# Optimization experiments

Measured on AMD Instinct MI355X. Metric: run time of the kernel, lower is better.

The kernel has to match this reference:

```python
import jax, jax.numpy as jnp
import numpy as np

N = 50000      # nodes
E = 1600000    # edges (avg degree 32)
F_IN = 256     # input feature dim
H = 128        # hidden == output size of GCN
C = 40         # num_class


def setup_inputs() -> dict:
    key = jax.random.key(0)
    ks = jax.random.split(key, 13)
    inp = {
        "features": jax.random.normal(ks[0], (N, F_IN), dtype=jnp.float32),
        "src": jax.random.randint(ks[1], (E,), 0, N, dtype=jnp.int32),
        "dst": jax.random.randint(ks[2], (E,), 0, N, dtype=jnp.int32),
        "edge_weight": jax.random.uniform(ks[3], (E,), dtype=jnp.float32),
        "y": jax.random.normal(ks[4], (N, C), dtype=jnp.float32),
        # GCN layer 1
        "W1": jax.random.normal(ks[5], (F_IN, H), dtype=jnp.float32) / np.sqrt(F_IN),
        "b1": jnp.zeros((H,), dtype=jnp.float32),
        # GCN layer 2
        "W2": jax.random.normal(ks[6], (H, H), dtype=jnp.float32) / np.sqrt(H),
        "b2": jnp.zeros((H,), dtype=jnp.float32),
        # y_fc_emb: Linear(num_class, output_size)
        "We": jax.random.normal(ks[7], (C, H), dtype=jnp.float32) / np.sqrt(C),
        "be": jnp.zeros((H,), dtype=jnp.float32),
        # y_fc: Linear(hidden*2, num_class)
        "Wf": jax.random.normal(ks[8], (2 * H, C), dtype=jnp.float32) / np.sqrt(2 * H),
        "bf": jnp.zeros((C,), dtype=jnp.float32),
    }
    return inp


def _spmm(edge_weight, src, dst, x, n):
    # (sparse adj) @ x : out[i] = sum_{(j->i)} w_ji * x[j]
    return jax.ops.segment_sum(edge_weight[:, None] * x[src], dst, num_segments=n)


def reference(features, src, dst, edge_weight, y, W1, b1, W2, b2, We, be, Wf, bf):
    n = features.shape[0]
    # F.normalize: L2 row-normalize with eps=1e-12 clamp
    norm = jnp.maximum(jnp.linalg.norm(features, axis=1, keepdims=True), 1e-12)
    x = features / norm
    # GCN layer 1: relu(adj @ (x @ W1) + b1)   (dropout = 0)
    h = jax.nn.relu(_spmm(edge_weight, src, dst, x @ W1, n) + b1)
    # GCN layer 2: adj @ (h @ W2) + b2
    h = _spmm(edge_weight, src, dst, h @ W2, n) + b2
    # label embedding + head
    y_emb = y @ We + be
    logits = jnp.concatenate([y_emb, h], axis=1) @ Wf + bf
    return jax.nn.softmax(logits, axis=-1)
```

## Files before the change

kernel.cpp:

```cpp
#include <hip/hip_runtime.h>
#include <hip/hip_bf16.h>
#include <hip/hip_fp16.h>
#include <cstdint>
#include <cstddef>
#include <cmath>

#define F_IN 256
#define HDIM 128
#define CCLS 40
#define NBMAX 1024
#define EPB_H 16384

typedef short bf16x8 __attribute__((ext_vector_type(8)));
typedef float f32x4 __attribute__((ext_vector_type(4)));

__device__ inline unsigned pkbf(float a, float b) {
  __hip_bfloat162 h = __float22bfloat162_rn(make_float2(a, b));
  unsigned u;
  __builtin_memcpy(&u, &h, 4);
  return u;
}
__device__ inline unsigned short bfr(float f) {
  __hip_bfloat16 h = __float2bfloat16(f);
  unsigned short u;
  __builtin_memcpy(&u, &h, 2);
  return u;
}
__device__ inline float f16tof(unsigned short hb) {
  __half hv;
  __builtin_memcpy(&hv, &hb, 2);
  return __half2float(hv);
}
__device__ inline unsigned short ftof16(float f) {
  __half hv = __float2half(f);
  unsigned short u;
  __builtin_memcpy(&u, &hv, 2);
  return u;
}

__global__ __launch_bounds__(256) void prep_kernel(const float* __restrict__ x,
                                                   unsigned short* __restrict__ featbf,
                                                   const float* __restrict__ W1,
                                                   const float* __restrict__ W2,
                                                   unsigned short* __restrict__ W1T,
                                                   unsigned short* __restrict__ W2T,
                                                   const float* __restrict__ We,
                                                   const float* __restrict__ be,
                                                   const float* __restrict__ Wf,
                                                   const float* __restrict__ bf,
                                                   float* __restrict__ Wc,
                                                   float* __restrict__ bc,
                                                   const int* __restrict__ dst,
                                                   int* __restrict__ gcount,
                                                   int n, int e, int nb) {
  const int b = blockIdx.x;
  const int t = threadIdx.x;
  const int nblk = (n + 15) >> 4;
  if (b < nblk) {
    const int wv = t >> 6, l = t & 63;
    const int r0 = b * 16 + wv * 4;
    const bool q0 = r0 < n, q1 = r0 + 1 < n, q2 = r0 + 2 < n, q3 = r0 + 3 < n;
    const float* p = x + (size_t)r0 * F_IN + l * 4;
    float4 z = make_float4(0.f, 0.f, 0.f, 0.f);
    float4 v0 = q0 ? *(const float4*)(p) : z;
    float4 v1 = q1 ? *(const float4*)(p + F_IN) : z;
    float4 v2 = q2 ? *(const float4*)(p + 2 * F_IN) : z;
    float4 v3 = q3 ? *(const float4*)(p + 3 * F_IN) : z;
    float s0 = v0.x * v0.x + v0.y * v0.y + v0.z * v0.z + v0.w * v0.w;
    float s1 = v1.x * v1.x + v1.y * v1.y + v1.z * v1.z + v1.w * v1.w;
    float s2 = v2.x * v2.x + v2.y * v2.y + v2.z * v2.z + v2.w * v2.w;
    float s3 = v3.x * v3.x + v3.y * v3.y + v3.z * v3.z + v3.w * v3.w;
#pragma unroll
    for (int off = 32; off; off >>= 1) {
      s0 += __shfl_xor(s0, off, 64);
      s1 += __shfl_xor(s1, off, 64);
      s2 += __shfl_xor(s2, off, 64);
      s3 += __shfl_xor(s3, off, 64);
    }
    float i0 = 1.0f / fmaxf(sqrtf(s0), 1e-12f);
    float i1 = 1.0f / fmaxf(sqrtf(s1), 1e-12f);
    float i2 = 1.0f / fmaxf(sqrtf(s2), 1e-12f);
    float i3 = 1.0f / fmaxf(sqrtf(s3), 1e-12f);
    unsigned short* o = featbf + (size_t)r0 * F_IN + l * 4;
    if (q0) *(uint2*)(o) = make_uint2(pkbf(v0.x * i0, v0.y * i0), pkbf(v0.z * i0, v0.w * i0));
    if (q1) *(uint2*)(o + F_IN) = make_uint2(pkbf(v1.x * i1, v1.y * i1), pkbf(v1.z * i1, v1.w * i1));
    if (q2) *(uint2*)(o + 2 * F_IN) = make_uint2(pkbf(v2.x * i2, v2.y * i2), pkbf(v2.z * i2, v2.w * i2));
    if (q3) *(uint2*)(o + 3 * F_IN) = make_uint2(pkbf(v3.x * i3, v3.y * i3), pkbf(v3.z * i3, v3.w * i3));
  } else if (b < nblk + 192) {
    int idx = (b - nblk) * 256 + t;
    if (idx < 128 * 256) {
      int nr = idx >> 8, k = idx & 255;
      W1T[idx] = bfr(W1[k * 128 + nr]);
    } else {
      int i2 = idx - 128 * 256;
      if (i2 < 128 * 128) {
        int nr = i2 >> 7, k = i2 & 127;
        W2T[i2] = bfr(W2[k * 128 + nr]);
      }
    }
  } else if (b < nblk + 194) {
    int part = b - (nblk + 192);
    int lo = part * 800, hi = lo + 800;
    for (int i = lo + t; i < hi; i += 256) {
      int c = i / CCLS, j = i % CCLS;
      float s = 0.f;
      for (int f = 0; f < HDIM; ++f) s += We[c * HDIM + f] * Wf[f * CCLS + j];
      Wc[i] = s;
    }
    if (part == 0 && t < CCLS) {
      float s = bf[t];
      for (int f = 0; f < HDIM; ++f) s += be[f] * Wf[f * CCLS + t];
      bc[t] = s;
    }
  } else {
    __shared__ int h[NBMAX];
    for (int i = t; i < nb; i += 256) h[i] = 0;
    __syncthreads();
    int b4 = (b - (nblk + 194)) * (EPB_H / 4);
#pragma unroll
    for (int k = 0; k < EPB_H / 1024; ++k) {
      int gi = b4 + k * 256 + t;
      int e0 = gi * 4;
      int4 d = make_int4(-1, -1, -1, -1);
      if (e0 + 3 < e) d = ((const int4*)dst)[gi];
      else if (e0 < e) {
        d.x = dst[e0];
        if (e0 + 1 < e) d.y = dst[e0 + 1];
        if (e0 + 2 < e) d.z = dst[e0 + 2];
      }
      if (d.x >= 0) atomicAdd(&h[d.x >> 6], 1);
      if (d.y >= 0) atomicAdd(&h[d.y >> 6], 1);
      if (d.z >= 0) atomicAdd(&h[d.z >> 6], 1);
      if (d.w >= 0) atomicAdd(&h[d.w >> 6], 1);
    }
    __syncthreads();
    for (int i = t; i < nb; i += 256)
      if (h[i]) atomicAdd(&gcount[i], h[i]);
  }
}

#define EPB 8192
__global__ __launch_bounds__(256) void bucket_scatter(const int* __restrict__ src,
                                                      const int* __restrict__ dst,
                                                      const float* __restrict__ w,
                                                      const int* __restrict__ gcount,
                                                      int* __restrict__ gcursor,
                                                      uint2* __restrict__ ews, int e, int nb) {
  __shared__ int hist[NBMAX];
  __shared__ int sb[NBMAX];
  __shared__ int lcur[NBMAX];
  __shared__ int part[256];
  const int t = threadIdx.x;
  for (int i = t; i < nb; i += 256) { hist[i] = 0; lcur[i] = 0; }
  __syncthreads();
  const int b4 = blockIdx.x * 2048;
  int4 dv[8];
#pragma unroll
  for (int k = 0; k < 8; ++k) {
    int gi = b4 + k * 256 + t;
    int e0 = gi * 4;
    int4 d = make_int4(-1, -1, -1, -1);
    if (e0 + 3 < e) d = ((const int4*)dst)[gi];
    else if (e0 < e) {
      d.x = dst[e0];
      if (e0 + 1 < e) d.y = dst[e0 + 1];
      if (e0 + 2 < e) d.z = dst[e0 + 2];
    }
    dv[k] = d;
    if (d.x >= 0) atomicAdd(&hist[d.x >> 6], 1);
    if (d.y >= 0) atomicAdd(&hist[d.y >> 6], 1);
    if (d.z >= 0) atomicAdd(&hist[d.z >> 6], 1);
    if (d.w >= 0) atomicAdd(&hist[d.w >> 6], 1);
  }
  __syncthreads();
  int v[4];
  int s = 0;
#pragma unroll
  for (int k = 0; k < 4; ++k) {
    int i = t * 4 + k;
    v[k] = (i < nb) ? gcount[i] : 0;
    s += v[k];
  }
  part[t] = s;
  __syncthreads();
  for (int off = 1; off < 256; off <<= 1) {
    int x = part[t];
    if (t >= off) x += part[t - off];
    __syncthreads();
    part[t] = x;
    __syncthreads();
  }
  int run = (t == 0) ? 0 : part[t - 1];
#pragma unroll
  for (int k = 0; k < 4; ++k) {
    int i = t * 4 + k;
    if (i < nb) sb[i] = run;
    run += v[k];
  }
  __syncthreads();
  for (int i = t; i < nb; i += 256) {
    int c = hist[i];
    sb[i] = sb[i] + (c ? atomicAdd(&gcursor[i], c) : 0);
  }
  __syncthreads();
#pragma unroll
  for (int k = 0; k < 8; ++k) {
    int gi = b4 + k * 256 + t;
    int e0 = gi * 4;
    if (e0 >= e) continue;
    int4 s4 = make_int4(0, 0, 0, 0);
    float4 w4 = make_float4(0.f, 0.f, 0.f, 0.f);
    if (e0 + 3 < e) { s4 = ((const int4*)src)[gi]; w4 = ((const float4*)w)[gi]; }
    else {
      s4.x = src[e0]; w4.x = w[e0];
      if (e0 + 1 < e) { s4.y = src[e0 + 1]; w4.y = w[e0 + 1]; }
      if (e0 + 2 < e) { s4.z = src[e0 + 2]; w4.z = w[e0 + 2]; }
    }
    int4 d = dv[k];
    if (d.x >= 0) { int bb = d.x >> 6; int r = atomicAdd(&lcur[bb], 1);
      ews[sb[bb] + r] = make_uint2(((unsigned)(d.x & 63) << 26) | (unsigned)s4.x, __float_as_uint(w4.x)); }
    if (d.y >= 0) { int bb = d.y >> 6; int r = atomicAdd(&lcur[bb], 1);
      ews[sb[bb] + r] = make_uint2(((unsigned)(d.y & 63) << 26) | (unsigned)s4.y, __float_as_uint(w4.y)); }
    if (d.z >= 0) { int bb = d.z >> 6; int r = atomicAdd(&lcur[bb], 1);
      ews[sb[bb] + r] = make_uint2(((unsigned)(d.z & 63) << 26) | (unsigned)s4.z, __float_as_uint(w4.z)); }
    if (d.w >= 0) { int bb = d.w >> 6; int r = atomicAdd(&lcur[bb], 1);
      ews[sb[bb] + r] = make_uint2(((unsigned)(d.w & 63) << 26) | (unsigned)s4.w, __float_as_uint(w4.w)); }
  }
}

__global__ __launch_bounds__(256) void bucket_sort(const uint2* __restrict__ ews,
                                                   const int* __restrict__ gcount,
                                                   unsigned* __restrict__ ews2,
                                                   int* __restrict__ row_off,
                                                   int n, int nb) {
  __shared__ int cnt64[64];
  __shared__ int cur[64];
  __shared__ int sred[4];
  const int t = threadIdx.x;
  const int b = blockIdx.x;
  int partial = 0;
  for (int i = t; i < b; i += 256) partial += gcount[i];
#pragma unroll
  for (int off = 32; off; off >>= 1) partial += __shfl_xor(partial, off, 64);
  if ((t & 63) == 0) sred[t >> 6] = partial;
  if (t < 64) cnt64[t] = 0;
  __syncthreads();
  const int e0 = sred[0] + sred[1] + sred[2] + sred[3];
  const int e1 = e0 + gcount[b];
  for (int i = e0 + t; i < e1; i += 256) atomicAdd(&cnt64[(unsigned)ews[i].x >> 26], 1);
  __syncthreads();
  if (t == 0) {
    int run = 0;
    for (int d = 0; d < 64; ++d) {
      int c = cnt64[d];
      cur[d] = run;
      run += c;
    }
  }
  __syncthreads();
  if (t < 64) {
    int node = b * 64 + t;
    if (node < n) row_off[node] = e0 + cur[t];
  }
  if (b == nb - 1 && t == 0) row_off[n] = e1;
  __syncthreads();
  for (int i = e0 + t; i < e1; i += 256) {
    uint2 p = ews[i];
    int d = (unsigned)p.x >> 26;
    int pos = e0 + atomicAdd(&cur[d], 1);
    unsigned rec = (p.x & 0xFFFFu) | ((unsigned)ftof16(__uint_as_float(p.y)) << 16);
    ews2[pos] = rec;
  }
}

#define SPMM_PAIR(ua, ub)                                                      \
  {                                                                            \
    unsigned u = half ? (ub) : (ua);                                           \
    float wt = f16tof((unsigned short)(u >> 16));                              \
    const uint2 xv = *(const uint2*)(xin + (size_t)(u & 0xFFFFu) * HDIM + fo); \
    acc.x = fmaf(wt, __uint_as_float(xv.x << 16), acc.x);                      \
    acc.y = fmaf(wt, __uint_as_float(xv.x & 0xFFFF0000u), acc.y);              \
    acc.z = fmaf(wt, __uint_as_float(xv.y << 16), acc.z);                      \
    acc.w = fmaf(wt, __uint_as_float(xv.y & 0xFFFF0000u), acc.w);              \
  }

template <int OUT_BF16>
__global__ __launch_bounds__(256) void spmm_bf16(const unsigned short* __restrict__ xin,
                                                 const unsigned* __restrict__ ews,
                                                 const int* __restrict__ row_off,
                                                 const float* __restrict__ bias,
                                                 void* __restrict__ outp, int n,
                                                 int do_relu) {
  const int t = threadIdx.x;
  const int l = t & 63;
  const int node = blockIdx.x * 4 + (t >> 6);
  if (node >= n) return;
  const int ue0 = __builtin_amdgcn_readfirstlane(row_off[node]);
  const int ue1 = __builtin_amdgcn_readfirstlane(row_off[node + 1]);
  const int cnt = ue1 - ue0;
  const unsigned* ep = ews + ue0;
  const int fo = (l & 31) * 4;
  const int half = l >> 5;
  float4 acc = make_float4(0.f, 0.f, 0.f, 0.f);

  int k = 0;
  for (; k + 16 <= cnt; k += 16) {
    unsigned a0 = ep[k + 0], a1 = ep[k + 1], a2 = ep[k + 2], a3 = ep[k + 3];
    unsigned a4 = ep[k + 4], a5 = ep[k + 5], a6 = ep[k + 6], a7 = ep[k + 7];
    unsigned a8 = ep[k + 8], a9 = ep[k + 9], a10 = ep[k + 10], a11 = ep[k + 11];
    unsigned a12 = ep[k + 12], a13 = ep[k + 13], a14 = ep[k + 14], a15 = ep[k + 15];
    SPMM_PAIR(a0, a1);
    SPMM_PAIR(a2, a3);
    SPMM_PAIR(a4, a5);
    SPMM_PAIR(a6, a7);
    SPMM_PAIR(a8, a9);
    SPMM_PAIR(a10, a11);
    SPMM_PAIR(a12, a13);
    SPMM_PAIR(a14, a15);
  }
  for (; k + 8 <= cnt; k += 8) {
    unsigned a0 = ep[k + 0], a1 = ep[k + 1], a2 = ep[k + 2], a3 = ep[k + 3];
    unsigned a4 = ep[k + 4], a5 = ep[k + 5], a6 = ep[k + 6], a7 = ep[k + 7];
    SPMM_PAIR(a0, a1);
    SPMM_PAIR(a2, a3);
    SPMM_PAIR(a4, a5);
    SPMM_PAIR(a6, a7);
  }
  for (; k < cnt; k += 2) {
    unsigned a0 = ep[k];
    unsigned a1 = (k + 1 < cnt) ? ep[k + 1] : 0u;
    SPMM_PAIR(a0, a1);
  }

  acc.x += __shfl_xor(acc.x, 32, 64);
  acc.y += __shfl_xor(acc.y, 32, 64);
  acc.z += __shfl_xor(acc.z, 32, 64);
  acc.w += __shfl_xor(acc.w, 32, 64);
  if (l < 32) {
    float4 bv = *(const float4*)(bias + fo);
    float4 r = make_float4(acc.x + bv.x, acc.y + bv.y, acc.z + bv.z, acc.w + bv.w);
    if (do_relu) {
      r.x = fmaxf(r.x, 0.f); r.y = fmaxf(r.y, 0.f);
      r.z = fmaxf(r.z, 0.f); r.w = fmaxf(r.w, 0.f);
    }
    if (OUT_BF16) {
      uint2 o = make_uint2(pkbf(r.x, r.y), pkbf(r.z, r.w));
      *(uint2*)((unsigned short*)outp + (size_t)node * HDIM + fo) = o;
    } else {
      *(float4*)((float*)outp + (size_t)node * HDIM + fo) = r;
    }
  }
}

template <int K>
__global__ __launch_bounds__(256) void gemm_mfma(const unsigned short* __restrict__ A,
                                                 const unsigned short* __restrict__ WT,
                                                 unsigned short* __restrict__ C, int M) {
  const int t = threadIdx.x;
  const int w = t >> 6, l = t & 63;
  const int ln = l & 15, quad = l >> 4;
  const int m0 = blockIdx.x * 64 + w * 16;
  const int arow = m0 + ln;
  const unsigned short* aptr = A + (size_t)(arow < M ? arow : (M - 1)) * K + quad * 8;

  f32x4 acc[8];
#pragma unroll
  for (int i = 0; i < 8; ++i) acc[i] = (f32x4){0.f, 0.f, 0.f, 0.f};

#pragma unroll
  for (int k0 = 0; k0 < K; k0 += 32) {
    bf16x8 af = *(const bf16x8*)(aptr + k0);
#pragma unroll
    for (int ti = 0; ti < 8; ++ti) {
      bf16x8 bf = *(const bf16x8*)(WT + (size_t)(ti * 16 + ln) * K + k0 + quad * 8);
      acc[ti] = __builtin_amdgcn_mfma_f32_16x16x32_bf16(af, bf, acc[ti], 0, 0, 0);
    }
  }

#pragma unroll
  for (int r = 0; r < 4; ++r) {
    int grow = m0 + quad * 4 + r;
    if (grow < M) {
      unsigned short* cp = C + (size_t)grow * HDIM + ln;
#pragma unroll
      for (int ti = 0; ti < 8; ++ti) cp[ti * 16] = bfr(acc[ti][r]);
    }
  }
}

__global__ __launch_bounds__(64) void head_kernel(const float* __restrict__ y,
                                                  const float* __restrict__ h2,
                                                  const float* __restrict__ Wc,
                                                  const float* __restrict__ bc,
                                                  const float* __restrict__ Wf,
                                                  float* __restrict__ out, int n) {
  __shared__ float sW[169 * CCLS];
  const int t = threadIdx.x;
  for (int i = t; i < 400; i += 64) ((float4*)sW)[i] = ((const float4*)Wc)[i];
  for (int i = t; i < 1280; i += 64)
    ((float4*)(sW + CCLS * CCLS))[i] = ((const float4*)(Wf + HDIM * CCLS))[i];
  if (t < 10) ((float4*)(sW + 168 * CCLS))[t] = ((const float4*)bc)[t];
  __syncthreads();

  const int node = blockIdx.x * 64 + t;
  const int nc = node < n ? node : n - 1;
  const float* zy = y + (size_t)nc * CCLS;
  const float* zh = h2 + (size_t)nc * HDIM;

  float acc[40];
#pragma unroll
  for (int cq = 0; cq < 10; ++cq) {
    float4 b4 = *(const float4*)&sW[168 * CCLS + cq * 4];
    acc[cq * 4 + 0] = b4.x; acc[cq * 4 + 1] = b4.y;
    acc[cq * 4 + 2] = b4.z; acc[cq * 4 + 3] = b4.w;
  }

#pragma unroll 2
  for (int kc = 0; kc < 10; ++kc) {
    float4 zv = *(const float4*)(zy + kc * 4);
    float zj[4] = {zv.x, zv.y, zv.z, zv.w};
#pragma unroll
    for (int j = 0; j < 4; ++j) {
      const float* wr = sW + (kc * 4 + j) * CCLS;
#pragma unroll
      for (int cq = 0; cq < 10; ++cq) {
        float4 w4 = *(const float4*)(wr + cq * 4);
        acc[cq * 4 + 0] = fmaf(zj[j], w4.x, acc[cq * 4 + 0]);
        acc[cq * 4 + 1] = fmaf(zj[j], w4.y, acc[cq * 4 + 1]);
        acc[cq * 4 + 2] = fmaf(zj[j], w4.z, acc[cq * 4 + 2]);
        acc[cq * 4 + 3] = fmaf(zj[j], w4.w, acc[cq * 4 + 3]);
      }
    }
  }
#pragma unroll 2
  for (int kc = 0; kc < 32; ++kc) {
    float4 zv = *(const float4*)(zh + kc * 4);
    float zj[4] = {zv.x, zv.y, zv.z, zv.w};
#pragma unroll
    for (int j = 0; j < 4; ++j) {
      const float* wr = sW + (40 + kc * 4 + j) * CCLS;
#pragma unroll
      for (int cq = 0; cq < 10; ++cq) {
        float4 w4 = *(const float4*)(wr + cq * 4);
        acc[cq * 4 + 0] = fmaf(zj[j], w4.x, acc[cq * 4 + 0]);
        acc[cq * 4 + 1] = fmaf(zj[j], w4.y, acc[cq * 4 + 1]);
        acc[cq * 4 + 2] = fmaf(zj[j], w4.z, acc[cq * 4 + 2]);
        acc[cq * 4 + 3] = fmaf(zj[j], w4.w, acc[cq * 4 + 3]);
      }
    }
  }

  float m = acc[0];
#pragma unroll
  for (int c = 1; c < 40; ++c) m = fmaxf(m, acc[c]);
  float sum = 0.f;
#pragma unroll
  for (int c = 0; c < 40; ++c) { acc[c] = __expf(acc[c] - m); sum += acc[c]; }
  float inv = 1.0f / sum;
  if (node < n) {
    float* op = out + (size_t)node * CCLS;
#pragma unroll
    for (int cq = 0; cq < 10; ++cq) {
      float4 o = make_float4(acc[cq * 4 + 0] * inv, acc[cq * 4 + 1] * inv,
                             acc[cq * 4 + 2] * inv, acc[cq * 4 + 3] * inv);
      *(float4*)(op + cq * 4) = o;
    }
  }
}

extern "C" void kernel_launch(void* const* d_in, const int* in_sizes, int n_in,
                              void* d_out, int out_size, void* d_ws, size_t ws_size,
                              hipStream_t stream) {
  (void)n_in; (void)out_size; (void)ws_size;
  const float* features = (const float*)d_in[0];
  const int*   src      = (const int*)d_in[1];
  const int*   dst      = (const int*)d_in[2];
  const float* ew       = (const float*)d_in[3];
  const float* y        = (const float*)d_in[4];
  const float* W1       = (const float*)d_in[5];
  const float* b1       = (const float*)d_in[6];
  const float* W2       = (const float*)d_in[7];
  const float* b2       = (const float*)d_in[8];
  const float* We       = (const float*)d_in[9];
  const float* be       = (const float*)d_in[10];
  const float* Wf       = (const float*)d_in[11];
  const float* bf       = (const float*)d_in[12];
  float* out = (float*)d_out;

  const int n = in_sizes[0] / F_IN;
  const int e = in_sizes[1];
  const int nb = (n + 63) >> 6;

  char* w = (char*)d_ws;
  auto take = [&](size_t bytes) {
    char* p = w;
    w += (bytes + 255) & ~(size_t)255;
    return p;
  };
  int*   gz       = (int*)take((size_t)2 * nb * 4);
  int*   gcount   = gz;
  int*   gcursor  = gz + nb;
  int*   row_off  = (int*)take((size_t)(n + 1) * 4);
  uint2* ews      = (uint2*)take((size_t)e * 8);
  unsigned* ews2  = (unsigned*)take((size_t)(e + 16) * 4);
  unsigned short* featbf = (unsigned short*)take((size_t)n * F_IN * 2);
  unsigned short* bufH1  = (unsigned short*)take((size_t)n * HDIM * 2);
  unsigned short* bufH2  = (unsigned short*)take((size_t)n * HDIM * 2);
  float* bufS     = (float*)take((size_t)n * HDIM * 4);
  unsigned short* W1T = (unsigned short*)take((size_t)HDIM * F_IN * 2);
  unsigned short* W2T = (unsigned short*)take((size_t)HDIM * HDIM * 2);
  float* Wc       = (float*)take(CCLS * CCLS * 4);
  float* bc       = (float*)take(CCLS * 4);

  const int nblk = (n + 15) >> 4;
  const int hb = (e + EPB_H - 1) / EPB_H;
  hipMemsetAsync(gz, 0, (size_t)2 * nb * 4, stream);
  prep_kernel<<<nblk + 194 + hb, 256, 0, stream>>>(features, featbf, W1, W2, W1T, W2T,
                                                   We, be, Wf, bf, Wc, bc, dst, gcount,
                                                   n, e, nb);
  bucket_scatter<<<(e + EPB - 1) / EPB, 256, 0, stream>>>(src, dst, ew, gcount, gcursor,
                                                          ews, e, nb);
  bucket_sort<<<nb, 256, 0, stream>>>(ews, gcount, ews2, row_off, n, nb);

  gemm_mfma<F_IN><<<(n + 63) / 64, 256, 0, stream>>>(featbf, W1T, bufH1, n);
  spmm_bf16<1><<<(n + 3) / 4, 256, 0, stream>>>(bufH1, ews2, row_off, b1, bufH2, n, 1);
  gemm_mfma<HDIM><<<(n + 63) / 64, 256, 0, stream>>>(bufH2, W2T, bufH1, n);
  spmm_bf16<0><<<(n + 3) / 4, 256, 0, stream>>>(bufH1, ews2, row_off, b2, bufS, n, 0);
  head_kernel<<<(n + 63) / 64, 64, 0, stream>>>(y, bufS, Wc, bc, Wf, out, n);
}
```

Before: 370.9 us.

## Fuse row normalization into first GEMM and widen SpMM gathers to 16B

Moves the L2 row normalization and bf16 conversion out of the prep kernel and into a new GEMM kernel that normalizes 64 rows into shared memory before running MFMA. This drops the write and re-read of the bf16 feature buffer. The SpMM kernel now gives each wave four 16-lane groups that each process a different edge with 8 features per lane (16-byte loads), unrolled 32 edges deep, and then reduces across the groups. This gives more gathers in flight and wider loads, at the cost of more registers and a two-step shuffle reduction. The fused GEMM has no __syncthreads between the shared-memory writes and reads, but each wave only reads the rows it wrote itself.

```diff
diff --git a/kernel.cpp b/kernel.cpp
--- a/kernel.cpp
+++ b/kernel.cpp
@@ -38,9 +38,7 @@
   return u;
 }
 
-__global__ __launch_bounds__(256) void prep_kernel(const float* __restrict__ x,
-                                                   unsigned short* __restrict__ featbf,
-                                                   const float* __restrict__ W1,
+__global__ __launch_bounds__(256) void prep_kernel(const float* __restrict__ W1,
                                                    const float* __restrict__ W2,
                                                    unsigned short* __restrict__ W1T,
                                                    unsigned short* __restrict__ W2T,
@@ -52,42 +50,11 @@
                                                    float* __restrict__ bc,
                                                    const int* __restrict__ dst,
                                                    int* __restrict__ gcount,
-                                                   int n, int e, int nb) {
+                                                   int e, int nb) {
   const int b = blockIdx.x;
   const int t = threadIdx.x;
-  const int nblk = (n + 15) >> 4;
-  if (b < nblk) {
-    const int wv = t >> 6, l = t & 63;
-    const int r0 = b * 16 + wv * 4;
-    const bool q0 = r0 < n, q1 = r0 + 1 < n, q2 = r0 + 2 < n, q3 = r0 + 3 < n;
-    const float* p = x + (size_t)r0 * F_IN + l * 4;
-    float4 z = make_float4(0.f, 0.f, 0.f, 0.f);
-    float4 v0 = q0 ? *(const float4*)(p) : z;
-    float4 v1 = q1 ? *(const float4*)(p + F_IN) : z;
-    float4 v2 = q2 ? *(const float4*)(p + 2 * F_IN) : z;
-    float4 v3 = q3 ? *(const float4*)(p + 3 * F_IN) : z;
-    float s0 = v0.x * v0.x + v0.y * v0.y + v0.z * v0.z + v0.w * v0.w;
-    float s1 = v1.x * v1.x + v1.y * v1.y + v1.z * v1.z + v1.w * v1.w;
-    float s2 = v2.x * v2.x + v2.y * v2.y + v2.z * v2.z + v2.w * v2.w;
-    float s3 = v3.x * v3.x + v3.y * v3.y + v3.z * v3.z + v3.w * v3.w;
-#pragma unroll
-    for (int off = 32; off; off >>= 1) {
-      s0 += __shfl_xor(s0, off, 64);
-      s1 += __shfl_xor(s1, off, 64);
-      s2 += __shfl_xor(s2, off, 64);
-      s3 += __shfl_xor(s3, off, 64);
-    }
-    float i0 = 1.0f / fmaxf(sqrtf(s0), 1e-12f);
-    float i1 = 1.0f / fmaxf(sqrtf(s1), 1e-12f);
-    float i2 = 1.0f / fmaxf(sqrtf(s2), 1e-12f);
-    float i3 = 1.0f / fmaxf(sqrtf(s3), 1e-12f);
-    unsigned short* o = featbf + (size_t)r0 * F_IN + l * 4;
-    if (q0) *(uint2*)(o) = make_uint2(pkbf(v0.x * i0, v0.y * i0), pkbf(v0.z * i0, v0.w * i0));
-    if (q1) *(uint2*)(o + F_IN) = make_uint2(pkbf(v1.x * i1, v1.y * i1), pkbf(v1.z * i1, v1.w * i1));
-    if (q2) *(uint2*)(o + 2 * F_IN) = make_uint2(pkbf(v2.x * i2, v2.y * i2), pkbf(v2.z * i2, v2.w * i2));
-    if (q3) *(uint2*)(o + 3 * F_IN) = make_uint2(pkbf(v3.x * i3, v3.y * i3), pkbf(v3.z * i3, v3.w * i3));
-  } else if (b < nblk + 192) {
-    int idx = (b - nblk) * 256 + t;
+  if (b < 192) {
+    int idx = b * 256 + t;
     if (idx < 128 * 256) {
       int nr = idx >> 8, k = idx & 255;
       W1T[idx] = bfr(W1[k * 128 + nr]);
@@ -98,8 +65,8 @@
         W2T[i2] = bfr(W2[k * 128 + nr]);
       }
     }
-  } else if (b < nblk + 194) {
-    int part = b - (nblk + 192);
+  } else if (b < 194) {
+    int part = b - 192;
     int lo = part * 800, hi = lo + 800;
     for (int i = lo + t; i < hi; i += 256) {
       int c = i / CCLS, j = i % CCLS;
@@ -116,7 +83,7 @@
     __shared__ int h[NBMAX];
     for (int i = t; i < nb; i += 256) h[i] = 0;
     __syncthreads();
-    int b4 = (b - (nblk + 194)) * (EPB_H / 4);
+    int b4 = (b - 194) * (EPB_H / 4);
 #pragma unroll
     for (int k = 0; k < EPB_H / 1024; ++k) {
       int gi = b4 + k * 256 + t;
@@ -273,16 +240,17 @@
   }
 }
 
-#define SPMM_PAIR(ua, ub)                                                      \
-  {                                                                            \
-    unsigned u = half ? (ub) : (ua);                                           \
-    float wt = f16tof((unsigned short)(u >> 16));                              \
-    const uint2 xv = *(const uint2*)(xin + (size_t)(u & 0xFFFFu) * HDIM + fo); \
-    acc.x = fmaf(wt, __uint_as_float(xv.x << 16), acc.x);                      \
-    acc.y = fmaf(wt, __uint_as_float(xv.x & 0xFFFF0000u), acc.y);              \
-    acc.z = fmaf(wt, __uint_as_float(xv.y << 16), acc.z);                      \
-    acc.w = fmaf(wt, __uint_as_float(xv.y & 0xFFFF0000u), acc.w);              \
-  }
+#define SEL4(b0, b1, b2, b3) (g == 0 ? (b0) : g == 1 ? (b1) : g == 2 ? (b2) : (b3))
+
+#define FMA8(wt, v)                                                    \
+  acc[0] = fmaf(wt, __uint_as_float((v).x << 16), acc[0]);             \
+  acc[1] = fmaf(wt, __uint_as_float((v).x & 0xFFFF0000u), acc[1]);     \
+  acc[2] = fmaf(wt, __uint_as_float((v).y << 16), acc[2]);             \
+  acc[3] = fmaf(wt, __uint_as_float((v).y & 0xFFFF0000u), acc[3]);     \
+  acc[4] = fmaf(wt, __uint_as_float((v).z << 16), acc[4]);             \
+  acc[5] = fmaf(wt, __uint_as_float((v).z & 0xFFFF0000u), acc[5]);     \
+  acc[6] = fmaf(wt, __uint_as_float((v).w << 16), acc[6]);             \
+  acc[7] = fmaf(wt, __uint_as_float((v).w & 0xFFFF0000u), acc[7]);
 
 template <int OUT_BF16>
 __global__ __launch_bounds__(256) void spmm_bf16(const unsigned short* __restrict__ xin,
@@ -299,55 +267,125 @@
   const int ue1 = __builtin_amdgcn_readfirstlane(row_off[node + 1]);
   const int cnt = ue1 - ue0;
   const unsigned* ep = ews + ue0;
-  const int fo = (l & 31) * 4;
-  const int half = l >> 5;
-  float4 acc = make_float4(0.f, 0.f, 0.f, 0.f);
+  const int g = l >> 4;
+  const int li = l & 15;
+  const int fo = li * 8;
+  float acc[8] = {0.f, 0.f, 0.f, 0.f, 0.f, 0.f, 0.f, 0.f};
 
   int k = 0;
+  for (; k + 32 <= cnt; k += 32) {
+    unsigned rr[8];
+#pragma unroll
+    for (int q = 0; q < 8; ++q) {
+      unsigned c0 = ep[k + q * 4 + 0], c1 = ep[k + q * 4 + 1];
+      unsigned c2 = ep[k + q * 4 + 2], c3 = ep[k + q * 4 + 3];
+      rr[q] = SEL4(c0, c1, c2, c3);
+    }
+    uint4 vv[8];
+#pragma unroll
+    for (int q = 0; q < 8; ++q)
+      vv[q] = *(const uint4*)(xin + (size_t)(rr[q] & 0xFFFFu) * HDIM + fo);
+#pragma unroll
+    for (int q = 0; q < 8; ++q) {
+      float wt = f16tof((unsigned short)(rr[q] >> 16));
+      FMA8(wt, vv[q]);
+    }
+  }
   for (; k + 16 <= cnt; k += 16) {
-    unsigned a0 = ep[k + 0], a1 = ep[k + 1], a2 = ep[k + 2], a3 = ep[k + 3];
-    unsigned a4 = ep[k + 4], a5 = ep[k + 5], a6 = ep[k + 6], a7 = ep[k + 7];
-    unsigned a8 = ep[k + 8], a9 = ep[k + 9], a10 = ep[k + 10], a11 = ep[k + 11];
-    unsigned a12 = ep[k + 12], a13 = ep[k + 13], a14 = ep[k + 14], a15 = ep[k + 15];
-    SPMM_PAIR(a0, a1);
-    SPMM_PAIR(a2, a3);
-    SPMM_PAIR(a4, a5);
-    SPMM_PAIR(a6, a7);
-    SPMM_PAIR(a8, a9);
-    SPMM_PAIR(a10, a11);
-    SPMM_PAIR(a12, a13);
-    SPMM_PAIR(a14, a15);
-  }
-  for (; k + 8 <= cnt; k += 8) {
-    unsigned a0 = ep[k + 0], a1 = ep[k + 1], a2 = ep[k + 2], a3 = ep[k + 3];
-    unsigned a4 = ep[k + 4], a5 = ep[k + 5], a6 = ep[k + 6], a7 = ep[k + 7];
-    SPMM_PAIR(a0, a1);
-    SPMM_PAIR(a2, a3);
-    SPMM_PAIR(a4, a5);
-    SPMM_PAIR(a6, a7);
-  }
-  for (; k < cnt; k += 2) {
-    unsigned a0 = ep[k];
-    unsigned a1 = (k + 1 < cnt) ? ep[k + 1] : 0u;
-    SPMM_PAIR(a0, a1);
-  }
-
-  acc.x += __shfl_xor(acc.x, 32, 64);
-  acc.y += __shfl_xor(acc.y, 32, 64);
-  acc.z += __shfl_xor(acc.z, 32, 64);
-  acc.w += __shfl_xor(acc.w, 32, 64);
-  if (l < 32) {
-    float4 bv = *(const float4*)(bias + fo);
-    float4 r = make_float4(acc.x + bv.x, acc.y + bv.y, acc.z + bv.z, acc.w + bv.w);
+    unsigned rr[4];
+#pragma unroll
+    for (int q = 0; q < 4; ++q) {
+      unsigned c0 = ep[k + q * 4 + 0], c1 = ep[k + q * 4 + 1];
+      unsigned c2 = ep[k + q * 4 + 2], c3 = ep[k + q * 4 + 3];
+      rr[q] = SEL4(c0, c1, c2, c3);
+    }
+    uint4 vv[4];
+#pragma unroll
+    for (int q = 0; q < 4; ++q)
+      vv[q] = *(const uint4*)(xin + (size_t)(rr[q] & 0xFFFFu) * HDIM + fo);
+#pragma unroll
+    for (int q = 0; q < 4; ++q) {
+      float wt = f16tof((unsigned short)(rr[q] >> 16));
+      FMA8(wt, vv[q]);
+    }
+  }
+  for (; k < cnt; k += 4) {
+    int idx = k + g;
+    unsigned r = (idx < cnt) ? ep[idx] : 0u;
+    uint4 v = *(const uint4*)(xin + (size_t)(r & 0xFFFFu) * HDIM + fo);
+    float wt = f16tof((unsigned short)(r >> 16));
+    FMA8(wt, v);
+  }
+
+#pragma unroll
+  for (int j = 0; j < 8; ++j) {
+    acc[j] += __shfl_xor(acc[j], 16, 64);
+    acc[j] += __shfl_xor(acc[j], 32, 64);
+  }
+  if (g == 0) {
+    float4 b0 = *(const float4*)(bias + fo);
+    float4 b1 = *(const float4*)(bias + fo + 4);
+    float r0 = acc[0] + b0.x, r1 = acc[1] + b0.y, r2 = acc[2] + b0.z, r3 = acc[3] + b0.w;
+    float r4 = acc[4] + b1.x, r5 = acc[5] + b1.y, r6 = acc[6] + b1.z, r7 = acc[7] + b1.w;
     if (do_relu) {
-      r.x = fmaxf(r.x, 0.f); r.y = fmaxf(r.y, 0.f);
-      r.z = fmaxf(r.z, 0.f); r.w = fmaxf(r.w, 0.f);
+      r0 = fmaxf(r0, 0.f); r1 = fmaxf(r1, 0.f); r2 = fmaxf(r2, 0.f); r3 = fmaxf(r3, 0.f);
+      r4 = fmaxf(r4, 0.f); r5 = fmaxf(r5, 0.f); r6 = fmaxf(r6, 0.f); r7 = fmaxf(r7, 0.f);
     }
     if (OUT_BF16) {
-      uint2 o = make_uint2(pkbf(r.x, r.y), pkbf(r.z, r.w));
-      *(uint2*)((unsigned short*)outp + (size_t)node * HDIM + fo) = o;
+      uint4 o = make_uint4(pkbf(r0, r1), pkbf(r2, r3), pkbf(r4, r5), pkbf(r6, r7));
+      *(uint4*)((unsigned short*)outp + (size_t)node * HDIM + fo) = o;
     } else {
-      *(float4*)((float*)outp + (size_t)node * HDIM + fo) = r;
+      float* op = (float*)outp + (size_t)node * HDIM + fo;
+      *(float4*)op = make_float4(r0, r1, r2, r3);
+      *(float4*)(op + 4) = make_float4(r4, r5, r6, r7);
+    }
+  }
+}
+
+__global__ __launch_bounds__(256) void gemm1_fused(const float* __restrict__ X,
+                                                   const unsigned short* __restrict__ WT,
+                                                   unsigned short* __restrict__ C, int M) {
+  __shared__ unsigned short As[64][264];
+  const int t = threadIdx.x;
+  const int w = t >> 6, l = t & 63;
+  const int bm0 = blockIdx.x * 64;
+
+  for (int rr = 0; rr < 16; ++rr) {
+    int row = w * 16 + rr;
+    int grow = bm0 + row;
+    const float* p = X + (size_t)(grow < M ? grow : (M - 1)) * F_IN + l * 4;
+    float4 v = *(const float4*)p;
+    float s = v.x * v.x + v.y * v.y + v.z * v.z + v.w * v.w;
+#pragma unroll
+    for (int off = 32; off; off >>= 1) s += __shfl_xor(s, off, 64);
+    float inv = 1.0f / fmaxf(sqrtf(s), 1e-12f);
+    *(uint2*)&As[row][l * 4] =
+        make_uint2(pkbf(v.x * inv, v.y * inv), pkbf(v.z * inv, v.w * inv));
+  }
+
+  const int ln = l & 15, quad = l >> 4;
+  const int m0 = bm0 + w * 16;
+  f32x4 acc[8];
+#pragma unroll
+  for (int i = 0; i < 8; ++i) acc[i] = (f32x4){0.f, 0.f, 0.f, 0.f};
+
+#pragma unroll
+  for (int k0 = 0; k0 < F_IN; k0 += 32) {
+    bf16x8 af = *(const bf16x8*)&As[w * 16 + ln][k0 + quad * 8];
+#pragma unroll
+    for (int ti = 0; ti < 8; ++ti) {
+      bf16x8 bfv = *(const bf16x8*)(WT + (size_t)(ti * 16 + ln) * F_IN + k0 + quad * 8);
+      acc[ti] = __builtin_amdgcn_mfma_f32_16x16x32_bf16(af, bfv, acc[ti], 0, 0, 0);
+    }
+  }
+
+#pragma unroll
+  for (int r = 0; r < 4; ++r) {
+    int grow = m0 + quad * 4 + r;
+    if (grow < M) {
+      unsigned short* cp = C + (size_t)grow * HDIM + ln;
+#pragma unroll
+      for (int ti = 0; ti < 8; ++ti) cp[ti * 16] = bfr(acc[ti][r]);
     }
   }
 }
@@ -372,8 +410,8 @@
     bf16x8 af = *(const bf16x8*)(aptr + k0);
 #pragma unroll
     for (int ti = 0; ti < 8; ++ti) {
-      bf16x8 bf = *(const bf16x8*)(WT + (size_t)(ti * 16 + ln) * K + k0 + quad * 8);
-      acc[ti] = __builtin_amdgcn_mfma_f32_16x16x32_bf16(af, bf, acc[ti], 0, 0, 0);
+      bf16x8 bfv = *(const bf16x8*)(WT + (size_t)(ti * 16 + ln) * K + k0 + quad * 8);
+      acc[ti] = __builtin_amdgcn_mfma_f32_16x16x32_bf16(af, bfv, acc[ti], 0, 0, 0);
     }
   }
 
@@ -503,7 +541,6 @@
   int*   row_off  = (int*)take((size_t)(n + 1) * 4);
   uint2* ews      = (uint2*)take((size_t)e * 8);
   unsigned* ews2  = (unsigned*)take((size_t)(e + 16) * 4);
-  unsigned short* featbf = (unsigned short*)take((size_t)n * F_IN * 2);
   unsigned short* bufH1  = (unsigned short*)take((size_t)n * HDIM * 2);
   unsigned short* bufH2  = (unsigned short*)take((size_t)n * HDIM * 2);
   float* bufS     = (float*)take((size_t)n * HDIM * 4);
@@ -512,17 +549,15 @@
   float* Wc       = (float*)take(CCLS * CCLS * 4);
   float* bc       = (float*)take(CCLS * 4);
 
-  const int nblk = (n + 15) >> 4;
   const int hb = (e + EPB_H - 1) / EPB_H;
   hipMemsetAsync(gz, 0, (size_t)2 * nb * 4, stream);
-  prep_kernel<<<nblk + 194 + hb, 256, 0, stream>>>(features, featbf, W1, W2, W1T, W2T,
-                                                   We, be, Wf, bf, Wc, bc, dst, gcount,
-                                                   n, e, nb);
+  prep_kernel<<<194 + hb, 256, 0, stream>>>(W1, W2, W1T, W2T, We, be, Wf, bf, Wc, bc,
+                                            dst, gcount, e, nb);
   bucket_scatter<<<(e + EPB - 1) / EPB, 256, 0, stream>>>(src, dst, ew, gcount, gcursor,
                                                           ews, e, nb);
   bucket_sort<<<nb, 256, 0, stream>>>(ews, gcount, ews2, row_off, n, nb);
 
-  gemm_mfma<F_IN><<<(n + 63) / 64, 256, 0, stream>>>(featbf, W1T, bufH1, n);
+  gemm1_fused<<<(n + 63) / 64, 256, 0, stream>>>(features, W1T, bufH1, n);
   spmm_bf16<1><<<(n + 3) / 4, 256, 0, stream>>>(bufH1, ews2, row_off, b1, bufH2, n, 1);
   gemm_mfma<HDIM><<<(n + 63) / 64, 256, 0, stream>>>(bufH2, W2T, bufH1, n);
   spmm_bf16<0><<<(n + 3) / 4, 256, 0, stream>>>(bufH1, ews2, row_off, b2, bufS, n, 0);
```

Result: slower. 400.3 us (+7.9%).

## Fuse L2 row-normalization into first GEMM and split second SpMM into column chunks

Applied to the files above, without the earlier changes.

Row normalization and bf16 conversion of the features now happen inside the first GEMM kernel, which stages the normalized rows in shared memory. This removes the prep-kernel pass and the write and re-read of a bf16 feature buffer. The second SpMM is replaced by a kernel that splits the 128 columns into four 32-column chunks handled by separate blocks, with eight edges processed in parallel per wave. The chunked SpMM reads each edge list four times but issues more independent gathers per wave; the fused GEMM adds a shared-memory staging step with little overlap.

```diff
diff --git a/kernel.cpp b/kernel.cpp
--- a/kernel.cpp
+++ b/kernel.cpp
@@ -38,9 +38,7 @@
   return u;
 }
 
-__global__ __launch_bounds__(256) void prep_kernel(const float* __restrict__ x,
-                                                   unsigned short* __restrict__ featbf,
-                                                   const float* __restrict__ W1,
+__global__ __launch_bounds__(256) void prep_kernel(const float* __restrict__ W1,
                                                    const float* __restrict__ W2,
                                                    unsigned short* __restrict__ W1T,
                                                    unsigned short* __restrict__ W2T,
@@ -52,42 +50,11 @@
                                                    float* __restrict__ bc,
                                                    const int* __restrict__ dst,
                                                    int* __restrict__ gcount,
-                                                   int n, int e, int nb) {
+                                                   int e, int nb) {
   const int b = blockIdx.x;
   const int t = threadIdx.x;
-  const int nblk = (n + 15) >> 4;
-  if (b < nblk) {
-    const int wv = t >> 6, l = t & 63;
-    const int r0 = b * 16 + wv * 4;
-    const bool q0 = r0 < n, q1 = r0 + 1 < n, q2 = r0 + 2 < n, q3 = r0 + 3 < n;
-    const float* p = x + (size_t)r0 * F_IN + l * 4;
-    float4 z = make_float4(0.f, 0.f, 0.f, 0.f);
-    float4 v0 = q0 ? *(const float4*)(p) : z;
-    float4 v1 = q1 ? *(const float4*)(p + F_IN) : z;
-    float4 v2 = q2 ? *(const float4*)(p + 2 * F_IN) : z;
-    float4 v3 = q3 ? *(const float4*)(p + 3 * F_IN) : z;
-    float s0 = v0.x * v0.x + v0.y * v0.y + v0.z * v0.z + v0.w * v0.w;
-    float s1 = v1.x * v1.x + v1.y * v1.y + v1.z * v1.z + v1.w * v1.w;
-    float s2 = v2.x * v2.x + v2.y * v2.y + v2.z * v2.z + v2.w * v2.w;
-    float s3 = v3.x * v3.x + v3.y * v3.y + v3.z * v3.z + v3.w * v3.w;
-#pragma unroll
-    for (int off = 32; off; off >>= 1) {
-      s0 += __shfl_xor(s0, off, 64);
-      s1 += __shfl_xor(s1, off, 64);
-      s2 += __shfl_xor(s2, off, 64);
-      s3 += __shfl_xor(s3, off, 64);
-    }
-    float i0 = 1.0f / fmaxf(sqrtf(s0), 1e-12f);
-    float i1 = 1.0f / fmaxf(sqrtf(s1), 1e-12f);
-    float i2 = 1.0f / fmaxf(sqrtf(s2), 1e-12f);
-    float i3 = 1.0f / fmaxf(sqrtf(s3), 1e-12f);
-    unsigned short* o = featbf + (size_t)r0 * F_IN + l * 4;
-    if (q0) *(uint2*)(o) = make_uint2(pkbf(v0.x * i0, v0.y * i0), pkbf(v0.z * i0, v0.w * i0));
-    if (q1) *(uint2*)(o + F_IN) = make_uint2(pkbf(v1.x * i1, v1.y * i1), pkbf(v1.z * i1, v1.w * i1));
-    if (q2) *(uint2*)(o + 2 * F_IN) = make_uint2(pkbf(v2.x * i2, v2.y * i2), pkbf(v2.z * i2, v2.w * i2));
-    if (q3) *(uint2*)(o + 3 * F_IN) = make_uint2(pkbf(v3.x * i3, v3.y * i3), pkbf(v3.z * i3, v3.w * i3));
-  } else if (b < nblk + 192) {
-    int idx = (b - nblk) * 256 + t;
+  if (b < 192) {
+    int idx = b * 256 + t;
     if (idx < 128 * 256) {
       int nr = idx >> 8, k = idx & 255;
       W1T[idx] = bfr(W1[k * 128 + nr]);
@@ -98,8 +65,8 @@
         W2T[i2] = bfr(W2[k * 128 + nr]);
       }
     }
-  } else if (b < nblk + 194) {
-    int part = b - (nblk + 192);
+  } else if (b < 194) {
+    int part = b - 192;
     int lo = part * 800, hi = lo + 800;
     for (int i = lo + t; i < hi; i += 256) {
       int c = i / CCLS, j = i % CCLS;
@@ -116,7 +83,7 @@
     __shared__ int h[NBMAX];
     for (int i = t; i < nb; i += 256) h[i] = 0;
     __syncthreads();
-    int b4 = (b - (nblk + 194)) * (EPB_H / 4);
+    int b4 = (b - 194) * (EPB_H / 4);
 #pragma unroll
     for (int k = 0; k < EPB_H / 1024; ++k) {
       int gi = b4 + k * 256 + t;
@@ -352,6 +319,129 @@
   }
 }
 
+#define CFMA4(r, v)                                                    \
+  {                                                                    \
+    float wt = f16tof((unsigned short)((r) >> 16));                    \
+    acc.x = fmaf(wt, __uint_as_float((v).x << 16), acc.x);             \
+    acc.y = fmaf(wt, __uint_as_float((v).x & 0xFFFF0000u), acc.y);     \
+    acc.z = fmaf(wt, __uint_as_float((v).y << 16), acc.z);             \
+    acc.w = fmaf(wt, __uint_as_float((v).y & 0xFFFF0000u), acc.w);     \
+  }
+
+__global__ __launch_bounds__(256) void spmm_chunk4(const unsigned short* __restrict__ xin,
+                                                   const unsigned* __restrict__ ews,
+                                                   const int* __restrict__ row_off,
+                                                   const float* __restrict__ bias,
+                                                   float* __restrict__ outp, int n) {
+  const int t = threadIdx.x;
+  const int l = t & 63;
+  const int chunk = blockIdx.x & 3;
+  const int node = (blockIdx.x >> 2) * 4 + (t >> 6);
+  if (node >= n) return;
+  const int ue0 = __builtin_amdgcn_readfirstlane(row_off[node]);
+  const int ue1 = __builtin_amdgcn_readfirstlane(row_off[node + 1]);
+  const int cnt = ue1 - ue0;
+  const unsigned* ep = ews + ue0;
+  const int slot = l >> 3;
+  const int ci = (l & 7) * 4;
+  const unsigned short* xc = xin + chunk * 32 + ci;
+  float4 acc = make_float4(0.f, 0.f, 0.f, 0.f);
+
+  int k = 0;
+  for (; k + 32 <= cnt; k += 32) {
+    unsigned r0 = ep[k + slot],      r1 = ep[k + 8 + slot];
+    unsigned r2 = ep[k + 16 + slot], r3 = ep[k + 24 + slot];
+    uint2 v0 = *(const uint2*)(xc + (size_t)(r0 & 0xFFFFu) * HDIM);
+    uint2 v1 = *(const uint2*)(xc + (size_t)(r1 & 0xFFFFu) * HDIM);
+    uint2 v2 = *(const uint2*)(xc + (size_t)(r2 & 0xFFFFu) * HDIM);
+    uint2 v3 = *(const uint2*)(xc + (size_t)(r3 & 0xFFFFu) * HDIM);
+    CFMA4(r0, v0);
+    CFMA4(r1, v1);
+    CFMA4(r2, v2);
+    CFMA4(r3, v3);
+  }
+  for (; k + 16 <= cnt; k += 16) {
+    unsigned r0 = ep[k + slot], r1 = ep[k + 8 + slot];
+    uint2 v0 = *(const uint2*)(xc + (size_t)(r0 & 0xFFFFu) * HDIM);
+    uint2 v1 = *(const uint2*)(xc + (size_t)(r1 & 0xFFFFu) * HDIM);
+    CFMA4(r0, v0);
+    CFMA4(r1, v1);
+  }
+  for (; k < cnt; k += 8) {
+    int idx = k + slot;
+    unsigned r0 = (idx < cnt) ? ep[idx] : 0u;
+    uint2 v0 = *(const uint2*)(xc + (size_t)(r0 & 0xFFFFu) * HDIM);
+    CFMA4(r0, v0);
+  }
+
+  acc.x += __shfl_xor(acc.x, 8, 64);
+  acc.y += __shfl_xor(acc.y, 8, 64);
+  acc.z += __shfl_xor(acc.z, 8, 64);
+  acc.w += __shfl_xor(acc.w, 8, 64);
+  acc.x += __shfl_xor(acc.x, 16, 64);
+  acc.y += __shfl_xor(acc.y, 16, 64);
+  acc.z += __shfl_xor(acc.z, 16, 64);
+  acc.w += __shfl_xor(acc.w, 16, 64);
+  acc.x += __shfl_xor(acc.x, 32, 64);
+  acc.y += __shfl_xor(acc.y, 32, 64);
+  acc.z += __shfl_xor(acc.z, 32, 64);
+  acc.w += __shfl_xor(acc.w, 32, 64);
+  if (slot == 0) {
+    const int co = chunk * 32 + ci;
+    float4 bv = *(const float4*)(bias + co);
+    *(float4*)(outp + (size_t)node * HDIM + co) =
+        make_float4(acc.x + bv.x, acc.y + bv.y, acc.z + bv.z, acc.w + bv.w);
+  }
+}
+
+__global__ __launch_bounds__(256) void gemm1_fused(const float* __restrict__ X,
+                                                   const unsigned short* __restrict__ WT,
+                                                   unsigned short* __restrict__ C, int M) {
+  __shared__ unsigned short As[64][264];
+  const int t = threadIdx.x;
+  const int w = t >> 6, l = t & 63;
+  const int bm0 = blockIdx.x * 64;
+
+  for (int rr = 0; rr < 16; ++rr) {
+    int row = w * 16 + rr;
+    int grow = bm0 + row;
+    const float* p = X + (size_t)(grow < M ? grow : (M - 1)) * F_IN + l * 4;
+    float4 v = *(const float4*)p;
+    float s = v.x * v.x + v.y * v.y + v.z * v.z + v.w * v.w;
+#pragma unroll
+    for (int off = 32; off; off >>= 1) s += __shfl_xor(s, off, 64);
+    float inv = 1.0f / fmaxf(sqrtf(s), 1e-12f);
+    *(uint2*)&As[row][l * 4] =
+        make_uint2(pkbf(v.x * inv, v.y * inv), pkbf(v.z * inv, v.w * inv));
+  }
+
+  const int ln = l & 15, quad = l >> 4;
+  const int m0 = bm0 + w * 16;
+  f32x4 acc[8];
+#pragma unroll
+  for (int i = 0; i < 8; ++i) acc[i] = (f32x4){0.f, 0.f, 0.f, 0.f};
+
+#pragma unroll
+  for (int k0 = 0; k0 < F_IN; k0 += 32) {
+    bf16x8 af = *(const bf16x8*)&As[w * 16 + ln][k0 + quad * 8];
+#pragma unroll
+    for (int ti = 0; ti < 8; ++ti) {
+      bf16x8 bfv = *(const bf16x8*)(WT + (size_t)(ti * 16 + ln) * F_IN + k0 + quad * 8);
+      acc[ti] = __builtin_amdgcn_mfma_f32_16x16x32_bf16(af, bfv, acc[ti], 0, 0, 0);
+    }
+  }
+
+#pragma unroll
+  for (int r = 0; r < 4; ++r) {
+    int grow = m0 + quad * 4 + r;
+    if (grow < M) {
+      unsigned short* cp = C + (size_t)grow * HDIM + ln;
+#pragma unroll
+      for (int ti = 0; ti < 8; ++ti) cp[ti * 16] = bfr(acc[ti][r]);
+    }
+  }
+}
+
 template <int K>
 __global__ __launch_bounds__(256) void gemm_mfma(const unsigned short* __restrict__ A,
                                                  const unsigned short* __restrict__ WT,
@@ -372,8 +462,8 @@
     bf16x8 af = *(const bf16x8*)(aptr + k0);
 #pragma unroll
     for (int ti = 0; ti < 8; ++ti) {
-      bf16x8 bf = *(const bf16x8*)(WT + (size_t)(ti * 16 + ln) * K + k0 + quad * 8);
-      acc[ti] = __builtin_amdgcn_mfma_f32_16x16x32_bf16(af, bf, acc[ti], 0, 0, 0);
+      bf16x8 bfv = *(const bf16x8*)(WT + (size_t)(ti * 16 + ln) * K + k0 + quad * 8);
+      acc[ti] = __builtin_amdgcn_mfma_f32_16x16x32_bf16(af, bfv, acc[ti], 0, 0, 0);
     }
   }
 
@@ -503,7 +593,6 @@
   int*   row_off  = (int*)take((size_t)(n + 1) * 4);
   uint2* ews      = (uint2*)take((size_t)e * 8);
   unsigned* ews2  = (unsigned*)take((size_t)(e + 16) * 4);
-  unsigned short* featbf = (unsigned short*)take((size_t)n * F_IN * 2);
   unsigned short* bufH1  = (unsigned short*)take((size_t)n * HDIM * 2);
   unsigned short* bufH2  = (unsigned short*)take((size_t)n * HDIM * 2);
   float* bufS     = (float*)take((size_t)n * HDIM * 4);
@@ -512,19 +601,17 @@
   float* Wc       = (float*)take(CCLS * CCLS * 4);
   float* bc       = (float*)take(CCLS * 4);
 
-  const int nblk = (n + 15) >> 4;
   const int hb = (e + EPB_H - 1) / EPB_H;
   hipMemsetAsync(gz, 0, (size_t)2 * nb * 4, stream);
-  prep_kernel<<<nblk + 194 + hb, 256, 0, stream>>>(features, featbf, W1, W2, W1T, W2T,
-                                                   We, be, Wf, bf, Wc, bc, dst, gcount,
-                                                   n, e, nb);
+  prep_kernel<<<194 + hb, 256, 0, stream>>>(W1, W2, W1T, W2T, We, be, Wf, bf, Wc, bc,
+                                            dst, gcount, e, nb);
   bucket_scatter<<<(e + EPB - 1) / EPB, 256, 0, stream>>>(src, dst, ew, gcount, gcursor,
                                                           ews, e, nb);
   bucket_sort<<<nb, 256, 0, stream>>>(ews, gcount, ews2, row_off, n, nb);
 
-  gemm_mfma<F_IN><<<(n + 63) / 64, 256, 0, stream>>>(featbf, W1T, bufH1, n);
+  gemm1_fused<<<(n + 63) / 64, 256, 0, stream>>>(features, W1T, bufH1, n);
   spmm_bf16<1><<<(n + 3) / 4, 256, 0, stream>>>(bufH1, ews2, row_off, b1, bufH2, n, 1);
   gemm_mfma<HDIM><<<(n + 63) / 64, 256, 0, stream>>>(bufH2, W2T, bufH1, n);
-  spmm_bf16<0><<<(n + 3) / 4, 256, 0, stream>>>(bufH1, ews2, row_off, b2, bufS, n, 0);
+  spmm_chunk4<<<((n + 3) / 4) * 4, 256, 0, stream>>>(bufH1, ews2, row_off, b2, bufS, n);
   head_kernel<<<(n + 63) / 64, 64, 0, stream>>>(y, bufS, Wc, bc, Wf, out, n);
 }
```

New measurement: 407.4 us. +9.9%, slower.
